# Kernel optimization log

Measured on AMD Instinct MI355X. Metric: run time of the kernel, lower is better.

Reference implementation:

```python
import jax, jax.numpy as jnp
import numpy as np

B, N, F, DM, DMO, OM, L = 32, 64, 64, 128, 64, 128, 4
PRE_H, PRE_O, POST_H = 128, 64, 64
E = N * N
EPS = 1e-5


def swish(x):
    return x * jax.nn.sigmoid(x)


def bn_edges(x, g, b):
    # BatchNorm1d(num_features=E) applied to [B, E, D]: per-edge-channel stats over (batch, D)
    m = x.mean(axis=(0, 2), keepdims=True)
    v = x.var(axis=(0, 2), keepdims=True)
    return (x - m) / jnp.sqrt(v + EPS) * g[None, :, None] + b[None, :, None]


def setup_inputs():
    key = jax.random.key(0)
    ks = iter(jax.random.split(key, 64))

    def rn(shape, s=0.05):
        return jax.random.normal(next(ks), shape, dtype=jnp.float32) * s

    # fully-connected graph incl. self-loops (required by BatchNorm1d(n_nodes^2))
    src, dst = np.meshgrid(np.arange(N), np.arange(N), indexing='ij')
    edge_index = jnp.asarray(np.stack([src.reshape(-1), dst.reshape(-1)]), dtype=jnp.int32)
    return {
        'node_feature': rn((B, N, F), 1.0),
        'vectors': rn((B, N, OM), 1.0),
        'edge_index': edge_index,
        'msg_W1': rn((L, 2 * F, DM)), 'msg_b1': rn((L, DM)),
        'bn1_g': jnp.ones((L, E), jnp.float32), 'bn1_b': jnp.zeros((L, E), jnp.float32),
        'msg_W2': rn((L, DM, DM)), 'msg_b2': rn((L, DM)),
        'bn2_g': jnp.ones((L, E), jnp.float32), 'bn2_b': jnp.zeros((L, E), jnp.float32),
        'msg_W3': rn((L, DM, DM)), 'msg_b3': rn((L, DM)),
        'bn3_g': jnp.ones((L, E), jnp.float32), 'bn3_b': jnp.zeros((L, E), jnp.float32),
        'msg_W4': rn((L, DM, DMO)), 'msg_b4': rn((L, DMO)),
        'upd_W1': rn((L, OM + F + DMO, DM)), 'upd_b1': rn((L, DM)),
        'upd_W2': rn((L, DM, DM)), 'upd_b2': rn((L, DM)),
        'upd_W3': rn((L, DM, DM)), 'upd_b3': rn((L, DM)),
        'upd_W4': rn((L, DM, F)), 'upd_b4': rn((L, F)),
        'pre_W1': rn((F, PRE_H)), 'pre_b1': rn((PRE_H,)),
        'pre_W2': rn((PRE_H, PRE_H)), 'pre_b2': rn((PRE_H,)),
        'pre_W3': rn((PRE_H, PRE_H)), 'pre_b3': rn((PRE_H,)),
        'pre_W4': rn((PRE_H, PRE_O)), 'pre_b4': rn((PRE_O,)),
        'post_W1': rn((PRE_O, POST_H)), 'post_b1': rn((POST_H,)),
        'post_W2': rn((POST_H, 1)), 'post_b2': rn((1,)),
    }


def reference(node_feature, vectors, edge_index,
              msg_W1, msg_b1, bn1_g, bn1_b, msg_W2, msg_b2, bn2_g, bn2_b,
              msg_W3, msg_b3, bn3_g, bn3_b, msg_W4, msg_b4,
              upd_W1, upd_b1, upd_W2, upd_b2, upd_W3, upd_b3, upd_W4, upd_b4,
              pre_W1, pre_b1, pre_W2, pre_b2, pre_W3, pre_b3, pre_W4, pre_b4,
              post_W1, post_b1, post_W2, post_b2):
    src, dst = edge_index[0], edge_index[1]
    x = node_feature  # [B, N, F]
    v = vectors       # [B, N, OM]
    cnt = jax.ops.segment_sum(jnp.ones((E,), jnp.float32), dst, num_segments=N)
    inv_cnt = 1.0 / jnp.maximum(cnt, 1.0)
    for l in range(L):
        x_i = x[:, dst]  # [B, E, F] gather targets
        x_j = x[:, src]  # [B, E, F] gather sources
        h = swish(jnp.concatenate([x_i, x_j], -1) @ msg_W1[l] + msg_b1[l])
        h = bn_edges(h, bn1_g[l], bn1_b[l])
        h = bn_edges(swish(h @ msg_W2[l] + msg_b2[l]), bn2_g[l], bn2_b[l])
        h = bn_edges(swish(h @ msg_W3[l] + msg_b3[l]), bn3_g[l], bn3_b[l])
        m = swish(h @ msg_W4[l] + msg_b4[l])  # [B, E, DMO]
        agg = jax.ops.segment_sum(jnp.transpose(m, (1, 0, 2)), dst, num_segments=N)
        agg = jnp.transpose(agg, (1, 0, 2)) * inv_cnt[None, :, None]  # mean aggr, [B, N, DMO]
        u = jnp.concatenate([v, x, agg], -1)  # [B, N, OM+F+DMO]
        h = swish(u @ upd_W1[l] + upd_b1[l])
        h = swish(h @ upd_W2[l] + upd_b2[l])
        h = swish(h @ upd_W3[l] + upd_b3[l])
        x = x + swish(h @ upd_W4[l] + upd_b4[l])  # residual update
    h = swish(x @ pre_W1 + pre_b1)
    h = swish(h @ pre_W2 + pre_b2)
    h = swish(h @ pre_W3 + pre_b3)
    h = h @ pre_W4 + pre_b4
    c = swish(h @ post_W1 + post_b1) @ post_W2 + post_b2  # [B, N, 1]
    x3 = jnp.einsum('bnd,bn->bd', v, c[..., 0])           # coefficient-weighted vector sum
    return x3, v, c
```

## Files before the change

### kernel.cpp

```cpp
#include <hip/hip_runtime.h>
#include <hip/hip_bf16.h>

typedef unsigned short u16t;
typedef __attribute__((ext_vector_type(8))) short bf16x8;
typedef __attribute__((ext_vector_type(4))) float f32x4;

#define Bn 32
#define Nn 64
#define Fd 64
#define DMd 128
#define DMOd 64
#define OMd 128
#define En 4096

#define NTEN 36
#define TOTALC 1073217
#define HP 136
#define UP 264
#define XP 72
#define WSEG 131072

__device__ const int kOffs[NTEN + 1] = {
    0,        131072,   393216,   458752,   459264,   475648,   492032,   557568,
    558080,   574464,   590848,   656384,   656896,   673280,   689664,   722432,
    722688,   853760,   854272,   919808,   920320,   985856,   986368,   1019136,
    1019392,  1027584,  1027712,  1044096,  1044224,  1060608,  1060736,  1068928,
    1068992,  1073088,  1073152,  1073216,  1073217
};

#define C_NF    0
#define C_VEC   131072
#define C_MW1   393216
#define C_MB1   458752
#define C_G1    459264
#define C_BB1   475648
#define C_MW2   492032
#define C_MB2   557568
#define C_G2    558080
#define C_BB2   574464
#define C_MW3   590848
#define C_MB3   656384
#define C_G3    656896
#define C_BB3   673280
#define C_MW4   689664
#define C_MB4   722432
#define C_UW1   722688
#define C_UB1   853760
#define C_UW2   854272
#define C_UB2   919808
#define C_UW3   920320
#define C_UB3   985856
#define C_UW4   986368
#define C_UB4   1019136
#define C_PW1   1019392
#define C_PB1   1027584
#define C_PW2   1027712
#define C_PB2   1044096
#define C_PW3   1044224
#define C_PB3   1060608
#define C_PW4   1060736
#define C_PB4   1068928
#define C_QW1   1068992
#define C_QB1   1073088
#define C_QW2   1073152
#define C_QB2   1073216

#define S_W2T 0
#define S_W3T 16384
#define S_W4T 32768
#define S_U1T 40960
#define S_U2T 73728
#define S_U3T 90112
#define S_U4T 106496
#define S_W1T 114688

struct Ptrs { const void* p[NTEN]; };

__device__ __forceinline__ float us2f(u16t u) {
    return __uint_as_float(((unsigned int)u) << 16);
}
__device__ __forceinline__ u16t f2us(float f) {
    __hip_bfloat16 h = __float2bfloat16(f);
    return *reinterpret_cast<u16t*>(&h);
}
__device__ __forceinline__ float swishf(float x) {
    return x * __builtin_amdgcn_rcpf(1.0f + __expf(-x));
}

__global__ void k_flag(const u16t* __restrict__ g1raw, int* __restrict__ flag) {
    if (threadIdx.x == 0) *flag = (g1raw[0] == 0x3F80u) ? 1 : 0;
}

__global__ __launch_bounds__(256) void k_convert(Ptrs t, float* __restrict__ C,
                                                 float* __restrict__ x,
                                                 const int* __restrict__ flagp) {
    int i = blockIdx.x * 256 + threadIdx.x;
    if (i >= TOTALC) return;
    const int flag = *flagp;
    int lo = 0, hi = NTEN;
    while (hi - lo > 1) { int m = (lo + hi) >> 1; if (i >= kOffs[m]) lo = m; else hi = m; }
    const int local = i - kOffs[lo];
    float v;
    if (flag) v = us2f(((const u16t*)t.p[lo])[local]);
    else      v = ((const float*)t.p[lo])[local];
    C[i] = v;
    if (i < Bn * Nn * Fd) x[i] = v;
}

__global__ __launch_bounds__(256) void k_prepw(const float* __restrict__ C,
                                               u16t* __restrict__ W) {
    int i = blockIdx.x * 256 + threadIdx.x;
    if (i >= 4 * WSEG) return;
    const int l = i / WSEG;
    int r = i - l * WSEG;
    int src;
    if (r < S_W3T)      { int q = r;          int n = q >> 7, k = q & 127; src = C_MW2 + l*16384 + k*128 + n; }
    else if (r < S_W4T) { int q = r - S_W3T;  int n = q >> 7, k = q & 127; src = C_MW3 + l*16384 + k*128 + n; }
    else if (r < S_U1T) { int q = r - S_W4T;  int n = q >> 7, k = q & 127; src = C_MW4 + l*8192  + k*64  + n; }
    else if (r < S_U2T) { int q = r - S_U1T;  int n = q >> 8, k = q & 255; src = C_UW1 + l*32768 + k*128 + n; }
    else if (r < S_U3T) { int q = r - S_U2T;  int n = q >> 7, k = q & 127; src = C_UW2 + l*16384 + k*128 + n; }
    else if (r < S_U4T) { int q = r - S_U3T;  int n = q >> 7, k = q & 127; src = C_UW3 + l*16384 + k*128 + n; }
    else if (r < S_W1T) { int q = r - S_U4T;  int n = q >> 7, k = q & 127; src = C_UW4 + l*8192  + k*64  + n; }
    else                { int q = r - S_W1T;  int n = q >> 7, k = q & 127; src = C_MW1 + l*16384 + k*128 + n; }
    W[i] = f2us(C[src]);
}

__global__ __launch_bounds__(128) void k_pq0(const float* __restrict__ x,
                                             const float* __restrict__ W1,
                                             float* __restrict__ P, float* __restrict__ Q,
                                             float* __restrict__ agg) {
    const int gid = blockIdx.x * 128 + threadIdx.x;
    if (gid < Bn * Nn * DMOd) agg[gid] = 0.f;
    __shared__ float xr[Fd];
    const int bn = blockIdx.x;
    const int tid = threadIdx.x;
    if (tid < Fd) xr[tid] = x[bn * Fd + tid];
    __syncthreads();
    float accP = 0.f, accQ = 0.f;
    #pragma unroll
    for (int k = 0; k < Fd; k++) {
        float xv = xr[k];
        accP += xv * W1[k * DMd + tid];
        accQ += xv * W1[(Fd + k) * DMd + tid];
    }
    P[bn * DMd + tid] = accP;
    Q[bn * DMd + tid] = accQ;
}

__device__ __forceinline__ void red8(float* s, float (*red)[8], float (*stats)[2],
                                     int wv, int lane, int tid) {
    #pragma unroll
    for (int off = 32; off > 0; off >>= 1)
        #pragma unroll
        for (int k = 0; k < 8; k++) s[k] += __shfl_down(s[k], off);
    if (lane == 0) {
        #pragma unroll
        for (int k = 0; k < 8; k++) red[wv][k] = s[k];
    }
    __syncthreads();
    if (tid < 4) {
        float S  = red[0][2*tid]   + red[1][2*tid]   + red[2][2*tid]   + red[3][2*tid];
        float S2 = red[0][2*tid+1] + red[1][2*tid+1] + red[2][2*tid+1] + red[3][2*tid+1];
        float mean = S * (1.0f / 4096.0f);
        float var  = S2 * (1.0f / 4096.0f) - mean * mean;
        stats[tid][0] = mean;
        stats[tid][1] = rsqrtf(var + 1e-5f);
    }
    __syncthreads();
}

__global__ __launch_bounds__(256, 3) void k_edge(
    const float* __restrict__ P, const float* __restrict__ Q,
    const float* __restrict__ b1v,
    const float* __restrict__ g1, const float* __restrict__ bb1,
    const u16t* __restrict__ W2t, const float* __restrict__ b2v,
    const float* __restrict__ g2, const float* __restrict__ bb2,
    const u16t* __restrict__ W3t, const float* __restrict__ b3v,
    const float* __restrict__ g3, const float* __restrict__ bb3,
    const u16t* __restrict__ W4t, const float* __restrict__ b4v,
    float* __restrict__ agg) {
    __shared__ u16t hE[4][Bn * HP];
    __shared__ float red[4][8];
    __shared__ float stats[4][2];

    const int dst = blockIdx.x & 63, src0 = (blockIdx.x >> 6) * 4;
    const int tid = threadIdx.x;
    const int wv = tid >> 6, lane = tid & 63, quad = lane >> 4, l15 = lane & 15;
    const int mw = wv & 1, nb2 = wv >> 1;
    const int mrow = mw * 16 + l15;
    const int nBase = nb2 * 64;

    {
        const int b = tid >> 3, d0 = (tid & 7) * 16;
        float4 pv[4], bv[4];
        {
            const float4* pp = (const float4*)&P[(b * Nn + dst) * DMd + d0];
            const float4* bp = (const float4*)&b1v[d0];
            #pragma unroll
            for (int j = 0; j < 4; j++) { pv[j] = pp[j]; bv[j] = bp[j]; }
        }
        float h[4][16];
        #pragma unroll
        for (int e = 0; e < 4; e++) {
            const float4* qq = (const float4*)&Q[(b * Nn + src0 + e) * DMd + d0];
            #pragma unroll
            for (int j = 0; j < 4; j++) {
                float4 qv = qq[j];
                h[e][j*4+0] = swishf(pv[j].x + qv.x + bv[j].x);
                h[e][j*4+1] = swishf(pv[j].y + qv.y + bv[j].y);
                h[e][j*4+2] = swishf(pv[j].z + qv.z + bv[j].z);
                h[e][j*4+3] = swishf(pv[j].w + qv.w + bv[j].w);
            }
        }
        float s[8];
        #pragma unroll
        for (int e = 0; e < 4; e++) {
            float se = 0.f, s2e = 0.f;
            #pragma unroll
            for (int i = 0; i < 16; i++) { se += h[e][i]; s2e += h[e][i] * h[e][i]; }
            s[2*e] = se; s[2*e+1] = s2e;
        }
        red8(s, red, stats, wv, lane, tid);
        #pragma unroll
        for (int e = 0; e < 4; e++) {
            float a  = stats[e][1] * g1[(src0 + e) * Nn + dst];
            float cc = bb1[(src0 + e) * Nn + dst] - stats[e][0] * a;
            bf16x8 s0, s1;
            #pragma unroll
            for (int j = 0; j < 8; j++) {
                s0[j] = (short)f2us(h[e][j] * a + cc);
                s1[j] = (short)f2us(h[e][8 + j] * a + cc);
            }
            *(bf16x8*)&hE[e][b * HP + d0]     = s0;
            *(bf16x8*)&hE[e][b * HP + d0 + 8] = s1;
        }
    }
    __syncthreads();

    #pragma unroll 1
    for (int st = 0; st < 2; st++) {
        const u16t*  Wt = st ? W3t : W2t;
        const float* bv = st ? b3v : b2v;
        const float* gv = st ? g3  : g2;
        const float* bb = st ? bb3 : bb2;
        f32x4 acc[4][4];
        #pragma unroll
        for (int t = 0; t < 4; t++) {
            float b0 = bv[nBase + t * 16 + l15];
            #pragma unroll
            for (int e = 0; e < 4; e++) acc[e][t] = (f32x4){b0, b0, b0, b0};
        }
        #pragma unroll
        for (int ks = 0; ks < 4; ks++) {
            bf16x8 wb[4];
            #pragma unroll
            for (int t = 0; t < 4; t++)
                wb[t] = *(const bf16x8*)&Wt[(nBase + t * 16 + l15) * 128 + ks * 32 + quad * 8];
            #pragma unroll
            for (int e = 0; e < 4; e++) {
                bf16x8 a8 = *(const bf16x8*)&hE[e][mrow * HP + ks * 32 + quad * 8];
                #pragma unroll
                for (int t = 0; t < 4; t++)
                    acc[e][t] = __builtin_amdgcn_mfma_f32_16x16x32_bf16(a8, wb[t], acc[e][t], 0, 0, 0);
            }
        }
        float s[8];
        #pragma unroll
        for (int e = 0; e < 4; e++) {
            float se = 0.f, s2e = 0.f;
            #pragma unroll
            for (int t = 0; t < 4; t++)
                #pragma unroll
                for (int r = 0; r < 4; r++) {
                    float v = swishf(acc[e][t][r]);
                    acc[e][t][r] = v;
                    se += v; s2e += v * v;
                }
            s[2*e] = se; s[2*e+1] = s2e;
        }
        red8(s, red, stats, wv, lane, tid);
        #pragma unroll
        for (int e = 0; e < 4; e++) {
            float a  = stats[e][1] * gv[(src0 + e) * Nn + dst];
            float cc = bb[(src0 + e) * Nn + dst] - stats[e][0] * a;
            #pragma unroll
            for (int t = 0; t < 4; t++)
                #pragma unroll
                for (int r = 0; r < 4; r++)
                    hE[e][(mw * 16 + quad * 4 + r) * HP + nBase + t * 16 + l15] =
                        f2us(acc[e][t][r] * a + cc);
        }
        __syncthreads();
    }

    {
        const int n40 = nb2 * 32;
        f32x4 a4[4][2];
        #pragma unroll
        for (int t = 0; t < 2; t++) {
            float b0 = b4v[n40 + t * 16 + l15];
            #pragma unroll
            for (int e = 0; e < 4; e++) a4[e][t] = (f32x4){b0, b0, b0, b0};
        }
        #pragma unroll
        for (int ks = 0; ks < 4; ks++) {
            bf16x8 wb[2];
            #pragma unroll
            for (int t = 0; t < 2; t++)
                wb[t] = *(const bf16x8*)&W4t[(n40 + t * 16 + l15) * 128 + ks * 32 + quad * 8];
            #pragma unroll
            for (int e = 0; e < 4; e++) {
                bf16x8 a8 = *(const bf16x8*)&hE[e][mrow * HP + ks * 32 + quad * 8];
                #pragma unroll
                for (int t = 0; t < 2; t++)
                    a4[e][t] = __builtin_amdgcn_mfma_f32_16x16x32_bf16(a8, wb[t], a4[e][t], 0, 0, 0);
            }
        }
        #pragma unroll
        for (int t = 0; t < 2; t++)
            #pragma unroll
            for (int r = 0; r < 4; r++) {
                float m = swishf(a4[0][t][r]) + swishf(a4[1][t][r])
                        + swishf(a4[2][t][r]) + swishf(a4[3][t][r]);
                int b = mw * 16 + quad * 4 + r;
                atomicAdd(&agg[(b * Nn + dst) * DMOd + n40 + t * 16 + l15], m);
            }
    }
}

__global__ __launch_bounds__(256, 4) void k_updq(
    const float* __restrict__ vC, float* __restrict__ x, float* __restrict__ agg,
    const u16t* __restrict__ U1t, const float* __restrict__ b1,
    const u16t* __restrict__ U2t, const float* __restrict__ b2,
    const u16t* __restrict__ U3t, const float* __restrict__ b3,
    const u16t* __restrict__ U4t, const float* __restrict__ b4,
    const u16t* __restrict__ W1Tn, float* __restrict__ Pn, float* __restrict__ Qn,
    int doPQ) {
    __shared__ u16t uL[16 * UP];
    __shared__ u16t hL[16 * HP];
    __shared__ u16t xL[16 * XP];
    const int g0 = blockIdx.x * 16;
    const int tid = threadIdx.x;
    const int wv = tid >> 6, lane = tid & 63, quad = lane >> 4, l15 = lane & 15;
    const int nBase = wv * 32;

    {
        const int i = tid >> 4, c0 = (tid & 15) * 16;
        const int g = g0 + i;
        const float* srcp; float scl = 1.f;
        if (c0 < 128)       srcp = &vC[g * OMd + c0];
        else if (c0 < 192)  srcp = &x[g * Fd + (c0 - 128)];
        else              { srcp = &agg[g * DMOd + (c0 - 192)]; scl = 1.0f / 64.0f; }
        bf16x8 s0, s1;
        #pragma unroll
        for (int j = 0; j < 8; j++) {
            s0[j] = (short)f2us(srcp[j] * scl);
            s1[j] = (short)f2us(srcp[8 + j] * scl);
        }
        *(bf16x8*)&uL[i * UP + c0]     = s0;
        *(bf16x8*)&uL[i * UP + c0 + 8] = s1;
    }
    __syncthreads();

    {
        f32x4 acc[2];
        #pragma unroll
        for (int t = 0; t < 2; t++) {
            float b0 = b1[nBase + t * 16 + l15];
            acc[t] = (f32x4){b0, b0, b0, b0};
        }
        #pragma unroll
        for (int ks = 0; ks < 8; ks++) {
            bf16x8 a8 = *(const bf16x8*)&uL[l15 * UP + ks * 32 + quad * 8];
            #pragma unroll
            for (int t = 0; t < 2; t++) {
                bf16x8 b8 = *(const bf16x8*)&U1t[(nBase + t * 16 + l15) * 256 + ks * 32 + quad * 8];
                acc[t] = __builtin_amdgcn_mfma_f32_16x16x32_bf16(a8, b8, acc[t], 0, 0, 0);
            }
        }
        #pragma unroll
        for (int t = 0; t < 2; t++)
            #pragma unroll
            for (int r = 0; r < 4; r++)
                hL[(quad * 4 + r) * HP + nBase + t * 16 + l15] = f2us(swishf(acc[t][r]));
    }
    __syncthreads();

    #pragma unroll 1
    for (int st = 0; st < 2; st++) {
        const u16t*  Ut = st ? U3t : U2t;
        const float* bb = st ? b3  : b2;
        f32x4 acc[2];
        #pragma unroll
        for (int t = 0; t < 2; t++) {
            float b0 = bb[nBase + t * 16 + l15];
            acc[t] = (f32x4){b0, b0, b0, b0};
        }
        #pragma unroll
        for (int ks = 0; ks < 4; ks++) {
            bf16x8 a8 = *(const bf16x8*)&hL[l15 * HP + ks * 32 + quad * 8];
            #pragma unroll
            for (int t = 0; t < 2; t++) {
                bf16x8 b8 = *(const bf16x8*)&Ut[(nBase + t * 16 + l15) * 128 + ks * 32 + quad * 8];
                acc[t] = __builtin_amdgcn_mfma_f32_16x16x32_bf16(a8, b8, acc[t], 0, 0, 0);
            }
        }
        __syncthreads();
        #pragma unroll
        for (int t = 0; t < 2; t++)
            #pragma unroll
            for (int r = 0; r < 4; r++)
                hL[(quad * 4 + r) * HP + nBase + t * 16 + l15] = f2us(swishf(acc[t][r]));
        __syncthreads();
    }

    {
        const int n4 = wv * 16;
        f32x4 acc;
        {
            float b0 = b4[n4 + l15];
            acc = (f32x4){b0, b0, b0, b0};
        }
        #pragma unroll
        for (int ks = 0; ks < 4; ks++) {
            bf16x8 a8 = *(const bf16x8*)&hL[l15 * HP + ks * 32 + quad * 8];
            bf16x8 b8 = *(const bf16x8*)&U4t[(n4 + l15) * 128 + ks * 32 + quad * 8];
            acc = __builtin_amdgcn_mfma_f32_16x16x32_bf16(a8, b8, acc, 0, 0, 0);
        }
        #pragma unroll
        for (int r = 0; r < 4; r++) {
            int row = quad * 4 + r, col = n4 + l15;
            float xn = x[(g0 + row) * Fd + col] + swishf(acc[r]);
            x[(g0 + row) * Fd + col] = xn;
            xL[row * XP + col] = f2us(xn);
        }
    }

    {
        int idx = tid;
        #pragma unroll
        for (int k = 0; k < 4; k++, idx += 256) agg[g0 * DMOd + idx] = 0.f;
    }
    __syncthreads();

    if (doPQ) {
        f32x4 ap[2], aq[2];
        #pragma unroll
        for (int j = 0; j < 2; j++) { ap[j] = (f32x4){0,0,0,0}; aq[j] = (f32x4){0,0,0,0}; }
        #pragma unroll
        for (int ks = 0; ks < 2; ks++) {
            bf16x8 a8 = *(const bf16x8*)&xL[l15 * XP + ks * 32 + quad * 8];
            #pragma unroll
            for (int j = 0; j < 2; j++) {
                const int n0 = (wv * 2 + j) * 16 + l15;
                bf16x8 bp = *(const bf16x8*)&W1Tn[n0 * 128 + ks * 32 + quad * 8];
                bf16x8 bq = *(const bf16x8*)&W1Tn[n0 * 128 + 64 + ks * 32 + quad * 8];
                ap[j] = __builtin_amdgcn_mfma_f32_16x16x32_bf16(a8, bp, ap[j], 0, 0, 0);
                aq[j] = __builtin_amdgcn_mfma_f32_16x16x32_bf16(a8, bq, aq[j], 0, 0, 0);
            }
        }
        #pragma unroll
        for (int j = 0; j < 2; j++)
            #pragma unroll
            for (int r = 0; r < 4; r++) {
                int g = g0 + quad * 4 + r, col = (wv * 2 + j) * 16 + l15;
                Pn[g * DMd + col] = ap[j][r];
                Qn[g * DMd + col] = aq[j][r];
            }
    }
}

__global__ __launch_bounds__(128) void k_final(
    const float* __restrict__ x, const void* __restrict__ vraw,
    const float* __restrict__ pW1, const float* __restrict__ pb1,
    const float* __restrict__ pW2, const float* __restrict__ pb2,
    const float* __restrict__ pW3, const float* __restrict__ pb3,
    const float* __restrict__ pW4, const float* __restrict__ pb4,
    const float* __restrict__ qW1, const float* __restrict__ qb1,
    const float* __restrict__ qW2, const float* __restrict__ qb2,
    float* __restrict__ c_buf, void* __restrict__ out, const int* __restrict__ flagp) {
    __shared__ float xr[64];
    __shared__ float ha[128];
    __shared__ float hb[128];
    __shared__ float hc[64];
    __shared__ float tt[64];
    const int bn = blockIdx.x;
    const int tid = threadIdx.x;
    const int flag = *flagp;
    if (tid < 64) xr[tid] = x[bn * Fd + tid];
    __syncthreads();
    float acc = pb1[tid];
    #pragma unroll 8
    for (int k = 0; k < 64; k++) acc += xr[k] * pW1[k * 128 + tid];
    ha[tid] = swishf(acc);
    __syncthreads();
    acc = pb2[tid];
    #pragma unroll 8
    for (int k = 0; k < 128; k++) acc += ha[k] * pW2[k * 128 + tid];
    hb[tid] = swishf(acc);
    __syncthreads();
    acc = pb3[tid];
    #pragma unroll 8
    for (int k = 0; k < 128; k++) acc += hb[k] * pW3[k * 128 + tid];
    ha[tid] = swishf(acc);
    __syncthreads();
    if (tid < 64) {
        acc = pb4[tid];
        #pragma unroll 8
        for (int k = 0; k < 128; k++) acc += ha[k] * pW4[k * 64 + tid];
        hc[tid] = acc;
    }
    __syncthreads();
    if (tid < 64) {
        acc = qb1[tid];
        #pragma unroll 8
        for (int k = 0; k < 64; k++) acc += hc[k] * qW1[k * 64 + tid];
        tt[tid] = swishf(acc);
    }
    __syncthreads();
    if (tid < 64) {
        float p = tt[tid] * qW2[tid];
        #pragma unroll
        for (int off = 32; off > 0; off >>= 1) p += __shfl_down(p, off);
        if (tid == 0) {
            float cv = p + qb2[0];
            c_buf[bn] = cv;
            const int ci = 4096 + Bn * Nn * OMd + bn;
            if (flag) ((u16t*)out)[ci] = f2us(cv);
            else      ((float*)out)[ci] = cv;
        }
    }
    const int vi = bn * OMd + tid;
    if (flag) ((u16t*)out)[4096 + vi] = ((const u16t*)vraw)[vi];
    else      ((float*)out)[4096 + vi] = ((const float*)vraw)[vi];
}

__global__ __launch_bounds__(128) void k_x3(const float* __restrict__ vC,
                                            const float* __restrict__ c_buf,
                                            void* __restrict__ out,
                                            const int* __restrict__ flagp) {
    const int b = blockIdx.x, d = threadIdx.x;
    const int flag = *flagp;
    float acc = 0.f;
    #pragma unroll 4
    for (int n = 0; n < Nn; n++)
        acc += vC[(b * Nn + n) * OMd + d] * c_buf[b * Nn + n];
    if (flag) ((u16t*)out)[b * OMd + d] = f2us(acc);
    else      ((float*)out)[b * OMd + d] = acc;
}

extern "C" void kernel_launch(void* const* d_in, const int* in_sizes, int n_in,
                              void* d_out, int out_size, void* d_ws, size_t ws_size,
                              hipStream_t stream) {
    float* ws = (float*)d_ws;
    int*   flag  = (int*)d_ws;
    float* C     = ws + 16;
    float* x     = C + 1073664;
    float* P     = x + 131072;
    float* Q     = P + 262144;
    float* agg   = Q + 262144;
    float* c_buf = agg + 131072;
    u16t*  Wt    = (u16t*)(c_buf + 2048);

    Ptrs t;
    for (int i = 0, j = 0; i < 37; i++) {
        if (i == 2) continue;
        t.p[j++] = d_in[i];
    }

    k_flag<<<1, 64, 0, stream>>>((const u16t*)d_in[5], flag);
    k_convert<<<(TOTALC + 255) / 256, 256, 0, stream>>>(t, C, x, flag);
    k_prepw<<<(4 * WSEG + 255) / 256, 256, 0, stream>>>(C, Wt);
    k_pq0<<<Bn * Nn, 128, 0, stream>>>(x, C + C_MW1, P, Q, agg);

    for (int l = 0; l < 4; l++) {
        u16t* Wl = Wt + l * WSEG;
        k_edge<<<64 * 16, 256, 0, stream>>>(
            P, Q,
            C + C_MB1 + l * DMd, C + C_G1 + l * En, C + C_BB1 + l * En,
            Wl + S_W2T, C + C_MB2 + l * DMd, C + C_G2 + l * En, C + C_BB2 + l * En,
            Wl + S_W3T, C + C_MB3 + l * DMd, C + C_G3 + l * En, C + C_BB3 + l * En,
            Wl + S_W4T, C + C_MB4 + l * DMOd,
            agg);
        const int doPQ = (l < 3) ? 1 : 0;
        const u16t* W1Tn = Wt + (doPQ ? (l + 1) : 0) * WSEG + S_W1T;
        k_updq<<<Bn * Nn / 16, 256, 0, stream>>>(
            C + C_VEC, x, agg,
            Wl + S_U1T, C + C_UB1 + l * DMd,
            Wl + S_U2T, C + C_UB2 + l * DMd,
            Wl + S_U3T, C + C_UB3 + l * DMd,
            Wl + S_U4T, C + C_UB4 + l * DMOd,
            W1Tn, P, Q, doPQ);
    }

    k_final<<<Bn * Nn, 128, 0, stream>>>(x, d_in[1],
        C + C_PW1, C + C_PB1, C + C_PW2, C + C_PB2,
        C + C_PW3, C + C_PB3, C + C_PW4, C + C_PB4,
        C + C_QW1, C + C_QB1, C + C_QW2, C + C_QB2,
        c_buf, d_out, flag);
    k_x3<<<Bn, 128, 0, stream>>>(C + C_VEC, c_buf, d_out, flag);
}
```

Baseline: 383.9 us.

## Fold BatchNorm affine into next GEMM epilogue via precomputed weight column sums

Instead of normalizing activations before writing them to LDS, the edge kernel now stores the raw swish outputs and applies the per-edge BN scale/shift after the following matmul, using precomputed column sums of each weight matrix (new k_cs kernel). This removes one block-wide sync per reduction and the separate normalize pass, and the MFMA operands are swapped so each lane writes packed 4-element bf16 rows to LDS. The risk is precision loss, since unnormalized values are rounded to bf16 and the column sums come from bf16-rounded weights.

```diff
diff --git a/kernel.cpp b/kernel.cpp
--- a/kernel.cpp
+++ b/kernel.cpp
@@ -3,6 +3,7 @@
 
 typedef unsigned short u16t;
 typedef __attribute__((ext_vector_type(8))) short bf16x8;
+typedef __attribute__((ext_vector_type(4))) short bf16x4;
 typedef __attribute__((ext_vector_type(4))) float f32x4;
 
 #define Bn 32
@@ -125,6 +126,21 @@
     W[i] = f2us(C[src]);
 }
 
+__global__ __launch_bounds__(256) void k_cs(const u16t* __restrict__ Wt,
+                                            float* __restrict__ CS) {
+    const int i = blockIdx.x * 256 + threadIdx.x;
+    if (i >= 4 * 320) return;
+    const int l = i / 320, j = i - l * 320;
+    const u16t* base = Wt + l * WSEG +
+        (j < 128 ? S_W2T + j * 128
+                 : (j < 256 ? S_W3T + (j - 128) * 128
+                            : S_W4T + (j - 256) * 128));
+    float s = 0.f;
+    #pragma unroll 8
+    for (int k = 0; k < 128; k++) s += us2f(base[k]);
+    CS[i] = s;
+}
+
 __global__ __launch_bounds__(128) void k_pq0(const float* __restrict__ x,
                                              const float* __restrict__ W1,
                                              float* __restrict__ P, float* __restrict__ Q,
@@ -147,41 +163,46 @@
     Q[bn * DMd + tid] = accQ;
 }
 
-__device__ __forceinline__ void red8(float* s, float (*red)[8], float (*stats)[2],
-                                     int wv, int lane, int tid) {
+__device__ __forceinline__ void wave_red8(float* s, float (*rd)[8], int wv, int lane) {
     #pragma unroll
     for (int off = 32; off > 0; off >>= 1)
         #pragma unroll
         for (int k = 0; k < 8; k++) s[k] += __shfl_down(s[k], off);
     if (lane == 0) {
         #pragma unroll
-        for (int k = 0; k < 8; k++) red[wv][k] = s[k];
-    }
-    __syncthreads();
-    if (tid < 4) {
-        float S  = red[0][2*tid]   + red[1][2*tid]   + red[2][2*tid]   + red[3][2*tid];
-        float S2 = red[0][2*tid+1] + red[1][2*tid+1] + red[2][2*tid+1] + red[3][2*tid+1];
+        for (int k = 0; k < 8; k++) rd[wv][k] = s[k];
+    }
+}
+
+__device__ __forceinline__ void calc_ab(const float (*rd)[8],
+                                        const float* __restrict__ g,
+                                        const float* __restrict__ bb,
+                                        int src0, int dst,
+                                        float* a, float* c) {
+    #pragma unroll
+    for (int e = 0; e < 4; e++) {
+        float S  = rd[0][2*e]   + rd[1][2*e]   + rd[2][2*e]   + rd[3][2*e];
+        float S2 = rd[0][2*e+1] + rd[1][2*e+1] + rd[2][2*e+1] + rd[3][2*e+1];
         float mean = S * (1.0f / 4096.0f);
         float var  = S2 * (1.0f / 4096.0f) - mean * mean;
-        stats[tid][0] = mean;
-        stats[tid][1] = rsqrtf(var + 1e-5f);
-    }
-    __syncthreads();
+        float av = rsqrtf(var + 1e-5f) * g[(src0 + e) * Nn + dst];
+        a[e] = av;
+        c[e] = bb[(src0 + e) * Nn + dst] - mean * av;
+    }
 }
 
 __global__ __launch_bounds__(256, 3) void k_edge(
     const float* __restrict__ P, const float* __restrict__ Q,
     const float* __restrict__ b1v,
     const float* __restrict__ g1, const float* __restrict__ bb1,
-    const u16t* __restrict__ W2t, const float* __restrict__ b2v,
+    const u16t* __restrict__ W2t, const float* __restrict__ b2v, const float* __restrict__ cs2,
     const float* __restrict__ g2, const float* __restrict__ bb2,
-    const u16t* __restrict__ W3t, const float* __restrict__ b3v,
+    const u16t* __restrict__ W3t, const float* __restrict__ b3v, const float* __restrict__ cs3,
     const float* __restrict__ g3, const float* __restrict__ bb3,
-    const u16t* __restrict__ W4t, const float* __restrict__ b4v,
+    const u16t* __restrict__ W4t, const float* __restrict__ b4v, const float* __restrict__ cs4,
     float* __restrict__ agg) {
     __shared__ u16t hE[4][Bn * HP];
-    __shared__ float red[4][8];
-    __shared__ float stats[4][2];
+    __shared__ float red[2][4][8];
 
     const int dst = blockIdx.x & 63, src0 = (blockIdx.x >> 6) * 4;
     const int tid = threadIdx.x;
@@ -192,64 +213,56 @@
 
     {
         const int b = tid >> 3, d0 = (tid & 7) * 16;
-        float4 pv[4], bv[4];
+        float4 pv[4], bv4[4];
         {
             const float4* pp = (const float4*)&P[(b * Nn + dst) * DMd + d0];
             const float4* bp = (const float4*)&b1v[d0];
             #pragma unroll
-            for (int j = 0; j < 4; j++) { pv[j] = pp[j]; bv[j] = bp[j]; }
-        }
-        float h[4][16];
+            for (int j = 0; j < 4; j++) { pv[j] = pp[j]; bv4[j] = bp[j]; }
+        }
+        float s[8];
         #pragma unroll
         for (int e = 0; e < 4; e++) {
             const float4* qq = (const float4*)&Q[(b * Nn + src0 + e) * DMd + d0];
+            float u[16];
             #pragma unroll
             for (int j = 0; j < 4; j++) {
                 float4 qv = qq[j];
-                h[e][j*4+0] = swishf(pv[j].x + qv.x + bv[j].x);
-                h[e][j*4+1] = swishf(pv[j].y + qv.y + bv[j].y);
-                h[e][j*4+2] = swishf(pv[j].z + qv.z + bv[j].z);
-                h[e][j*4+3] = swishf(pv[j].w + qv.w + bv[j].w);
-            }
-        }
-        float s[8];
-        #pragma unroll
-        for (int e = 0; e < 4; e++) {
+                u[j*4+0] = swishf(pv[j].x + qv.x + bv4[j].x);
+                u[j*4+1] = swishf(pv[j].y + qv.y + bv4[j].y);
+                u[j*4+2] = swishf(pv[j].z + qv.z + bv4[j].z);
+                u[j*4+3] = swishf(pv[j].w + qv.w + bv4[j].w);
+            }
             float se = 0.f, s2e = 0.f;
             #pragma unroll
-            for (int i = 0; i < 16; i++) { se += h[e][i]; s2e += h[e][i] * h[e][i]; }
-            s[2*e] = se; s[2*e+1] = s2e;
-        }
-        red8(s, red, stats, wv, lane, tid);
-        #pragma unroll
-        for (int e = 0; e < 4; e++) {
-            float a  = stats[e][1] * g1[(src0 + e) * Nn + dst];
-            float cc = bb1[(src0 + e) * Nn + dst] - stats[e][0] * a;
+            for (int i = 0; i < 16; i++) { se += u[i]; s2e += u[i] * u[i]; }
             bf16x8 s0, s1;
             #pragma unroll
             for (int j = 0; j < 8; j++) {
-                s0[j] = (short)f2us(h[e][j] * a + cc);
-                s1[j] = (short)f2us(h[e][8 + j] * a + cc);
+                s0[j] = (short)f2us(u[j]);
+                s1[j] = (short)f2us(u[8 + j]);
             }
             *(bf16x8*)&hE[e][b * HP + d0]     = s0;
             *(bf16x8*)&hE[e][b * HP + d0 + 8] = s1;
-        }
-    }
-    __syncthreads();
+            s[2*e] = se; s[2*e+1] = s2e;
+        }
+        wave_red8(s, red[0], wv, lane);
+    }
+    __syncthreads();
+
+    float aP[4], cP[4];
+    calc_ab(red[0], g1, bb1, src0, dst, aP, cP);
 
     #pragma unroll 1
     for (int st = 0; st < 2; st++) {
         const u16t*  Wt = st ? W3t : W2t;
         const float* bv = st ? b3v : b2v;
-        const float* gv = st ? g3  : g2;
-        const float* bb = st ? bb3 : bb2;
+        const float* cv = st ? cs3 : cs2;
         f32x4 acc[4][4];
         #pragma unroll
-        for (int t = 0; t < 4; t++) {
-            float b0 = bv[nBase + t * 16 + l15];
-            #pragma unroll
-            for (int e = 0; e < 4; e++) acc[e][t] = (f32x4){b0, b0, b0, b0};
-        }
+        for (int e = 0; e < 4; e++)
+            #pragma unroll
+            for (int t = 0; t < 4; t++) acc[e][t] = (f32x4){0.f, 0.f, 0.f, 0.f};
         #pragma unroll
         for (int ks = 0; ks < 4; ks++) {
             bf16x8 wb[4];
@@ -261,35 +274,45 @@
                 bf16x8 a8 = *(const bf16x8*)&hE[e][mrow * HP + ks * 32 + quad * 8];
                 #pragma unroll
                 for (int t = 0; t < 4; t++)
-                    acc[e][t] = __builtin_amdgcn_mfma_f32_16x16x32_bf16(a8, wb[t], acc[e][t], 0, 0, 0);
-            }
+                    acc[e][t] = __builtin_amdgcn_mfma_f32_16x16x32_bf16(wb[t], a8, acc[e][t], 0, 0, 0);
+            }
+        }
+        float4 c4[4], bb4[4];
+        #pragma unroll
+        for (int t = 0; t < 4; t++) {
+            const int n0 = nBase + t * 16 + quad * 4;
+            c4[t]  = *(const float4*)&cv[n0];
+            bb4[t] = *(const float4*)&bv[n0];
         }
         float s[8];
         #pragma unroll
         for (int e = 0; e < 4; e++) {
+            const float ae = aP[e], ce = cP[e];
             float se = 0.f, s2e = 0.f;
             #pragma unroll
-            for (int t = 0; t < 4; t++)
+            for (int t = 0; t < 4; t++) {
                 #pragma unroll
                 for (int r = 0; r < 4; r++) {
-                    float v = swishf(acc[e][t][r]);
-                    acc[e][t][r] = v;
-                    se += v; s2e += v * v;
+                    float z = ae * acc[e][t][r] + (ce * (&c4[t].x)[r] + (&bb4[t].x)[r]);
+                    float u = swishf(z);
+                    acc[e][t][r] = u;
+                    se += u; s2e += u * u;
                 }
+            }
             s[2*e] = se; s[2*e+1] = s2e;
         }
-        red8(s, red, stats, wv, lane, tid);
-        #pragma unroll
-        for (int e = 0; e < 4; e++) {
-            float a  = stats[e][1] * gv[(src0 + e) * Nn + dst];
-            float cc = bb[(src0 + e) * Nn + dst] - stats[e][0] * a;
-            #pragma unroll
-            for (int t = 0; t < 4; t++)
+        wave_red8(s, red[1 - st], wv, lane);
+        __syncthreads();
+        calc_ab(red[1 - st], st ? g3 : g2, st ? bb3 : bb2, src0, dst, aP, cP);
+        #pragma unroll
+        for (int e = 0; e < 4; e++)
+            #pragma unroll
+            for (int t = 0; t < 4; t++) {
+                bf16x4 pk;
                 #pragma unroll
-                for (int r = 0; r < 4; r++)
-                    hE[e][(mw * 16 + quad * 4 + r) * HP + nBase + t * 16 + l15] =
-                        f2us(acc[e][t][r] * a + cc);
-        }
+                for (int r = 0; r < 4; r++) pk[r] = (short)f2us(acc[e][t][r]);
+                *(bf16x4*)&hE[e][mrow * HP + nBase + t * 16 + quad * 4] = pk;
+            }
         __syncthreads();
     }
 
@@ -297,10 +320,9 @@
         const int n40 = nb2 * 32;
         f32x4 a4[4][2];
         #pragma unroll
-        for (int t = 0; t < 2; t++) {
-            float b0 = b4v[n40 + t * 16 + l15];
-            #pragma unroll
-            for (int e = 0; e < 4; e++) a4[e][t] = (f32x4){b0, b0, b0, b0};
+        for (int e = 0; e < 4; e++) {
+            a4[e][0] = (f32x4){0.f, 0.f, 0.f, 0.f};
+            a4[e][1] = (f32x4){0.f, 0.f, 0.f, 0.f};
         }
         #pragma unroll
         for (int ks = 0; ks < 4; ks++) {
@@ -317,14 +339,22 @@
             }
         }
         #pragma unroll
-        for (int t = 0; t < 2; t++)
+        for (int t = 0; t < 2; t++) {
+            const int col = n40 + t * 16 + l15;
+            const float csv = cs4[col], bvv = b4v[col];
+            float fe[4];
+            #pragma unroll
+            for (int e = 0; e < 4; e++) fe[e] = cP[e] * csv + bvv;
             #pragma unroll
             for (int r = 0; r < 4; r++) {
-                float m = swishf(a4[0][t][r]) + swishf(a4[1][t][r])
-                        + swishf(a4[2][t][r]) + swishf(a4[3][t][r]);
-                int b = mw * 16 + quad * 4 + r;
-                atomicAdd(&agg[(b * Nn + dst) * DMOd + n40 + t * 16 + l15], m);
-            }
+                float m = swishf(aP[0] * a4[0][t][r] + fe[0])
+                        + swishf(aP[1] * a4[1][t][r] + fe[1])
+                        + swishf(aP[2] * a4[2][t][r] + fe[2])
+                        + swishf(aP[3] * a4[3][t][r] + fe[3]);
+                const int b = mw * 16 + quad * 4 + r;
+                atomicAdd(&agg[(b * Nn + dst) * DMOd + col], m);
+            }
+        }
     }
 }
 
@@ -561,6 +591,7 @@
     float* agg   = Q + 262144;
     float* c_buf = agg + 131072;
     u16t*  Wt    = (u16t*)(c_buf + 2048);
+    float* CS    = (float*)(Wt + 4 * WSEG);
 
     Ptrs t;
     for (int i = 0, j = 0; i < 37; i++) {
@@ -571,16 +602,20 @@
     k_flag<<<1, 64, 0, stream>>>((const u16t*)d_in[5], flag);
     k_convert<<<(TOTALC + 255) / 256, 256, 0, stream>>>(t, C, x, flag);
     k_prepw<<<(4 * WSEG + 255) / 256, 256, 0, stream>>>(C, Wt);
+    k_cs<<<5, 256, 0, stream>>>(Wt, CS);
     k_pq0<<<Bn * Nn, 128, 0, stream>>>(x, C + C_MW1, P, Q, agg);
 
     for (int l = 0; l < 4; l++) {
         u16t* Wl = Wt + l * WSEG;
+        float* CSl = CS + l * 320;
         k_edge<<<64 * 16, 256, 0, stream>>>(
             P, Q,
             C + C_MB1 + l * DMd, C + C_G1 + l * En, C + C_BB1 + l * En,
-            Wl + S_W2T, C + C_MB2 + l * DMd, C + C_G2 + l * En, C + C_BB2 + l * En,
-            Wl + S_W3T, C + C_MB3 + l * DMd, C + C_G3 + l * En, C + C_BB3 + l * En,
-            Wl + S_W4T, C + C_MB4 + l * DMOd,
+            Wl + S_W2T, C + C_MB2 + l * DMd, CSl,
+            C + C_G2 + l * En, C + C_BB2 + l * En,
+            Wl + S_W3T, C + C_MB3 + l * DMd, CSl + 128,
+            C + C_G3 + l * En, C + C_BB3 + l * En,
+            Wl + S_W4T, C + C_MB4 + l * DMOd, CSl + 256,
             agg);
         const int doPQ = (l < 3) ? 1 : 0;
         const u16t* W1Tn = Wt + (doPQ ? (l + 1) : 0) * WSEG + S_W1T;
```

Measured after the change: 377.6 us. About the same (-1.6%).
